# Optimization experiments

Measured on AMD Instinct MI355X. Metric: run time of the kernel, lower is better.

## Reference

```python
import jax, jax.numpy as jnp
import numpy as np

NUM_GROUPS = 8
EPS = 1e-6

def group_norm(x, gamma, beta):
    # x: [B, C, L]
    B, C, L = x.shape
    g = x.reshape(B, NUM_GROUPS, (C // NUM_GROUPS) * L)
    mean = g.mean(axis=-1, keepdims=True)
    var = g.var(axis=-1, keepdims=True)
    g = (g - mean) * jax.lax.rsqrt(var + EPS)
    g = g.reshape(B, C, L)
    return g * gamma[None, :, None] + beta[None, :, None]

def conv1x1(h, w, b):
    # w: [O, C], b: [O]; h: [B, C, L]
    return jnp.einsum('oc,bcl->bol', w, h) + b[None, :, None]

def setup_inputs() -> dict:
    key = jax.random.key(0)
    ks = jax.random.split(key, 12)
    B, C, L = 8, 512, 2048
    s = 1.0 / np.sqrt(C)
    inp = {
        'x': jax.random.normal(ks[0], (B, C, L), dtype=jnp.float32),
        'gamma': jnp.ones((C,), jnp.float32),
        'beta': jnp.zeros((C,), jnp.float32),
        'wq': jax.random.uniform(ks[1], (C, C), jnp.float32, -s, s),
        'bq': jax.random.uniform(ks[2], (C,), jnp.float32, -s, s),
        'wk': jax.random.uniform(ks[3], (C, C), jnp.float32, -s, s),
        'bk': jax.random.uniform(ks[4], (C,), jnp.float32, -s, s),
        'wv': jax.random.uniform(ks[5], (C, C), jnp.float32, -s, s),
        'bv': jax.random.uniform(ks[6], (C,), jnp.float32, -s, s),
        'wo': jax.random.uniform(ks[7], (C, C), jnp.float32, -s, s),
        'bo': jax.random.uniform(ks[8], (C,), jnp.float32, -s, s),
    }
    return inp

def reference(x, gamma, beta, wq, bq, wk, bk, wv, bv, wo, bo):
    C = x.shape[1]
    h = group_norm(x, gamma, beta)
    q = conv1x1(h, wq, bq)  # [B, C, L]
    k = conv1x1(h, wk, bk)
    v = conv1x1(h, wv, bv)
    # scores: [B, Lq, Lk] = q^T k, scaled by C^-0.5
    w = jnp.einsum('bci,bcj->bij', q, k) * (C ** -0.5)
    w = jax.nn.softmax(w, axis=2)
    # h[b,c,i] = sum_j v[b,c,j] * w[b,i,j]
    h = jnp.einsum('bcj,bij->bci', v, w)
    h = conv1x1(h, wo, bo)
    return x + h
```

## Files before the change

kernel.cpp:

```cpp
#include <hip/hip_runtime.h>
#include <hip/hip_bf16.h>
#include <cstdio>

typedef __attribute__((ext_vector_type(8))) short short8;
typedef __attribute__((ext_vector_type(8))) unsigned short ushort8;
typedef __attribute__((ext_vector_type(4))) float f32x4;
typedef __attribute__((ext_vector_type(4))) unsigned short ushort4v;

__device__ inline unsigned short f2bf(float f){
    unsigned int u = __float_as_uint(f);
    unsigned int r = (u + 0x7fffu + ((u >> 16) & 1u)) >> 16;
    return (unsigned short)r;
}
__device__ inline float bf2f(unsigned short b){
    return __uint_as_float((unsigned int)b << 16);
}

__device__ inline void store1(float* p, float v){ *p = v; }
__device__ inline void store1(unsigned short* p, float v){ *p = f2bf(v); }

#define GLDS(gp, lp) __builtin_amdgcn_global_load_lds( \
    (const __attribute__((address_space(1))) void*)(gp), \
    (__attribute__((address_space(3))) void*)(lp), 16, 0, 0)

#define WAITV(N) asm volatile("s_waitcnt vmcnt(" #N ")" ::: "memory")

#define MFMA_Q(ACC, AF, BF) \
    _Pragma("unroll") \
    for (int ks = 0; ks < 2; ks++) \
        _Pragma("unroll") \
        for (int mi = 0; mi < 4; mi++) \
            _Pragma("unroll") \
            for (int ni = 0; ni < 2; ni++) \
                ACC[mi * 2 + ni] = __builtin_amdgcn_mfma_f32_16x16x32_bf16( \
                    AF[ks][mi], BF[ks][ni], ACC[mi * 2 + ni], 0, 0, 0);

template<typename OutT, int EPI>
__global__ __launch_bounds__(512, 2)
void gemm256(const unsigned short* __restrict__ Ag,
             const unsigned short* __restrict__ Bg,
             OutT* __restrict__ Cg,
             int K, int lda, int ldb, int ldc,
             long sA, long sB, long sC,
             const float* __restrict__ bias,
             const float* __restrict__ resid, long sR,
             float scale)
{
    const int gx = gridDim.x, gy = gridDim.y;
    const int nwg  = gx * gy * (int)gridDim.z;
    const int orig = blockIdx.x + gx * (blockIdx.y + gy * blockIdx.z);
    const int cpx  = nwg >> 3;
    const int nid  = (orig & 7) * cpx + (orig >> 3);
    const int bx   = nid % gx;
    const int tmp  = nid / gx;
    const int by   = tmp % gy;
    const int bz   = tmp / gy;

    Ag += (long)bz * sA;
    Bg += (long)bz * sB;
    Cg += (long)bz * sC;
    const int m0 = by * 256;
    const int n0 = bx * 256;

    __shared__ unsigned short As[2][16384];
    __shared__ unsigned short Bs[2][16384];

    const int t    = threadIdx.x;
    const int wave = t >> 6;
    const int lane = t & 63;
    const int rg   = wave >> 2;
    const int cg   = wave & 3;
    const int wm   = rg * 128;
    const int wn   = cg * 64;
    const int lhi  = lane >> 4;
    const int llo  = lane & 15;

    f32x4 acc0[8], acc1[8], acc2[8], acc3[8];
#pragma unroll
    for (int f = 0; f < 8; f++){
        acc0[f] = (f32x4)(0.0f); acc1[f] = (f32x4)(0.0f);
        acc2[f] = (f32x4)(0.0f); acc3[f] = (f32x4)(0.0f);
    }

    const int s_rr = t >> 3, s_cb = t & 7;
    const int s_cs = s_cb ^ (s_rr & 7);
    auto stageA = [&](int bi, int k0, int j){
        GLDS(Ag + (long)(m0 + j * 64 + s_rr) * lda + k0 + s_cs * 8,
             &As[bi][j * 4096 + wave * 512]);
    };
    auto stageB = [&](int bi, int k0, int j){
        GLDS(Bg + (long)(n0 + j * 64 + s_rr) * ldb + k0 + s_cs * 8,
             &Bs[bi][j * 4096 + wave * 512]);
    };

    const int nt = K >> 6;
    stageB(0, 0, 0); stageB(0, 0, 1); stageB(0, 0, 2); stageB(0, 0, 3);
    stageA(0, 0, 0); stageA(0, 0, 2); stageA(0, 0, 1); stageA(0, 0, 3);
    WAITV(2);
    __builtin_amdgcn_s_barrier();
    __builtin_amdgcn_sched_barrier(0);

    int cur = 0;
    for (int kt = 0; kt < nt; kt++){
        const bool more = (kt + 1 < nt);
        const int nk0 = (kt + 1) << 6;
        short8 af[2][4], bf0[2][2], bf1[2][2];

#pragma unroll
        for (int ks = 0; ks < 2; ks++){
#pragma unroll
            for (int mi = 0; mi < 4; mi++){
                const int r  = wm + mi * 16 + llo;
                const int pc = (ks * 4 + lhi) ^ (r & 7);
                af[ks][mi] = *(const short8*)(&As[cur][r * 64 + pc * 8]);
            }
#pragma unroll
            for (int ni = 0; ni < 2; ni++){
                const int r  = wn + ni * 16 + llo;
                const int pc = (ks * 4 + lhi) ^ (r & 7);
                bf0[ks][ni] = *(const short8*)(&Bs[cur][r * 64 + pc * 8]);
            }
        }
        __builtin_amdgcn_sched_barrier(0);
        if (more){ stageB(cur ^ 1, nk0, 0); stageB(cur ^ 1, nk0, 1); }
        __builtin_amdgcn_s_barrier();
        __builtin_amdgcn_sched_barrier(0);
        __builtin_amdgcn_s_setprio(1);
        MFMA_Q(acc0, af, bf0);
        __builtin_amdgcn_s_setprio(0);
        __builtin_amdgcn_s_barrier();
        __builtin_amdgcn_sched_barrier(0);

#pragma unroll
        for (int ks = 0; ks < 2; ks++)
#pragma unroll
            for (int ni = 0; ni < 2; ni++){
                const int r  = wn + 32 + ni * 16 + llo;
                const int pc = (ks * 4 + lhi) ^ (r & 7);
                bf1[ks][ni] = *(const short8*)(&Bs[cur][r * 64 + pc * 8]);
            }
        __builtin_amdgcn_sched_barrier(0);
        if (more){ stageB(cur ^ 1, nk0, 2); stageB(cur ^ 1, nk0, 3); WAITV(4); }
        else     { WAITV(0); }
        __builtin_amdgcn_s_barrier();
        __builtin_amdgcn_sched_barrier(0);
        __builtin_amdgcn_s_setprio(1);
        MFMA_Q(acc1, af, bf1);
        __builtin_amdgcn_s_setprio(0);
        __builtin_amdgcn_s_barrier();
        __builtin_amdgcn_sched_barrier(0);

#pragma unroll
        for (int ks = 0; ks < 2; ks++)
#pragma unroll
            for (int mi = 0; mi < 4; mi++){
                const int r  = wm + 64 + mi * 16 + llo;
                const int pc = (ks * 4 + lhi) ^ (r & 7);
                af[ks][mi] = *(const short8*)(&As[cur][r * 64 + pc * 8]);
            }
        __builtin_amdgcn_sched_barrier(0);
        if (more){ stageA(cur ^ 1, nk0, 0); stageA(cur ^ 1, nk0, 2); }
        __builtin_amdgcn_s_barrier();
        __builtin_amdgcn_sched_barrier(0);
        __builtin_amdgcn_s_setprio(1);
        MFMA_Q(acc2, af, bf1);
        __builtin_amdgcn_s_setprio(0);
        __builtin_amdgcn_s_barrier();
        __builtin_amdgcn_sched_barrier(0);

        if (more){ stageA(cur ^ 1, nk0, 1); stageA(cur ^ 1, nk0, 3); WAITV(2); }
        __builtin_amdgcn_s_barrier();
        __builtin_amdgcn_sched_barrier(0);
        __builtin_amdgcn_s_setprio(1);
        MFMA_Q(acc3, af, bf0);
        __builtin_amdgcn_s_setprio(0);
        __builtin_amdgcn_s_barrier();
        __builtin_amdgcn_sched_barrier(0);

        cur ^= 1;
    }

    auto epi = [&](f32x4 (&A)[8], int h, int cl){
#pragma unroll
        for (int mi = 0; mi < 4; mi++){
#pragma unroll
            for (int ni = 0; ni < 2; ni++){
                const int n  = n0 + wn + cl * 32 + ni * 16 + llo;
                const int mb = m0 + wm + h * 64 + mi * 16 + lhi * 4;
                f32x4 v = A[mi * 2 + ni];
#pragma unroll
                for (int j = 0; j < 4; j++){
                    const int m = mb + j;
                    float val = v[j] * scale;
                    if (EPI == 1) val += bias[n];
                    if (EPI == 2) val += bias[m];
                    if (EPI == 3) val += bias[m] + resid[(long)bz * sR + (long)m * ldc + n];
                    store1(&Cg[(long)m * ldc + n], val);
                }
            }
        }
    };
    epi(acc0, 0, 0); epi(acc1, 0, 1); epi(acc2, 1, 1); epi(acc3, 1, 0);
}

template<typename OutT, int EPI>
__global__ __launch_bounds__(256)
void gemm_nt(const unsigned short* __restrict__ Ag,
             const unsigned short* __restrict__ Bg,
             OutT* __restrict__ Cg,
             int K, int lda, int ldb, int ldc,
             long sA, long sB, long sC,
             const float* __restrict__ bias,
             const float* __restrict__ resid, long sR,
             float scale)
{
    const int gx = gridDim.x, gy = gridDim.y;
    const int nwg  = gx * gy * (int)gridDim.z;
    const int orig = blockIdx.x + gx * (blockIdx.y + gy * blockIdx.z);
    const int cpx  = nwg >> 3;
    const int nid  = (orig & 7) * cpx + (orig >> 3);
    const int bx   = nid % gx;
    const int tmp  = nid / gx;
    const int by   = tmp % gy;
    const int bz   = tmp / gy;

    Ag += (long)bz * sA;
    Bg += (long)bz * sB;
    Cg += (long)bz * sC;
    const int m0 = by * 128;
    const int n0 = bx * 128;

    __shared__ unsigned short As[2][128 * 64];
    __shared__ unsigned short Bs[2][128 * 64];

    const int t    = threadIdx.x;
    const int wave = t >> 6;
    const int lane = t & 63;
    const int wm   = (wave >> 1) << 6;
    const int wn   = (wave & 1) << 6;
    const int lhi  = lane >> 4;
    const int llo  = lane & 15;

    f32x4 acc[4][4];
#pragma unroll
    for (int i = 0; i < 4; i++)
#pragma unroll
        for (int j = 0; j < 4; j++) acc[i][j] = (f32x4)(0.0f);

    auto stage = [&](int bi, int k0){
#pragma unroll
        for (int i = 0; i < 4; i++){
            const int tt = i * 256 + t;
            const int r  = tt >> 3;
            const int cb = tt & 7;
            const int cs = cb ^ (r & 7);
            GLDS(Ag + (long)(m0 + r) * lda + k0 + cs * 8, &As[bi][i * 2048 + wave * 512]);
            GLDS(Bg + (long)(n0 + r) * ldb + k0 + cs * 8, &Bs[bi][i * 2048 + wave * 512]);
        }
    };

    const int nt = K >> 6;
    stage(0, 0);
    __syncthreads();

    int cur = 0;
    for (int kt = 0; kt < nt; kt++){
        if (kt + 1 < nt) stage(cur ^ 1, (kt + 1) << 6);
#pragma unroll
        for (int ksub = 0; ksub < 2; ksub++){
            short8 af[4], bf[4];
#pragma unroll
            for (int mi = 0; mi < 4; mi++){
                const int r  = wm + mi * 16 + llo;
                const int cs = (ksub * 4 + lhi) ^ (r & 7);
                af[mi] = *(const short8*)(&As[cur][r * 64 + cs * 8]);
            }
#pragma unroll
            for (int ni = 0; ni < 4; ni++){
                const int r  = wn + ni * 16 + llo;
                const int cs = (ksub * 4 + lhi) ^ (r & 7);
                bf[ni] = *(const short8*)(&Bs[cur][r * 64 + cs * 8]);
            }
#pragma unroll
            for (int mi = 0; mi < 4; mi++)
#pragma unroll
                for (int ni = 0; ni < 4; ni++)
                    acc[mi][ni] = __builtin_amdgcn_mfma_f32_16x16x32_bf16(
                        af[mi], bf[ni], acc[mi][ni], 0, 0, 0);
        }
        __syncthreads();
        cur ^= 1;
    }

#pragma unroll
    for (int mi = 0; mi < 4; mi++){
#pragma unroll
        for (int ni = 0; ni < 4; ni++){
            const int n  = n0 + wn + ni * 16 + llo;
            const int mb = m0 + wm + mi * 16 + lhi * 4;
            f32x4 v = acc[mi][ni];
#pragma unroll
            for (int j = 0; j < 4; j++){
                const int m = mb + j;
                float val = v[j] * scale;
                if (EPI == 1) val += bias[n];
                if (EPI == 2) val += bias[m];
                if (EPI == 3) val += bias[m] + resid[(long)bz * sR + (long)m * ldc + n];
                store1(&Cg[(long)m * ldc + n], val);
            }
        }
    }
}


__global__ void gn_partial(const float* __restrict__ x, float* __restrict__ part){
    const long base = (long)blockIdx.x * 8192;
    const float4* xp = (const float4*)(x + base);
    float s = 0.f, ss = 0.f;
    for (int i = threadIdx.x; i < 2048; i += 256){
        float4 v = xp[i];
        s  += (v.x + v.y) + (v.z + v.w);
        ss += (v.x * v.x + v.y * v.y) + (v.z * v.z + v.w * v.w);
    }
    for (int o = 32; o; o >>= 1){ s += __shfl_down(s, o); ss += __shfl_down(ss, o); }
    __shared__ float rs[4], rss[4];
    const int wave = threadIdx.x >> 6, lane = threadIdx.x & 63;
    if (lane == 0){ rs[wave] = s; rss[wave] = ss; }
    __syncthreads();
    if (threadIdx.x == 0){
        part[blockIdx.x * 2]     = (rs[0] + rs[1]) + (rs[2] + rs[3]);
        part[blockIdx.x * 2 + 1] = (rss[0] + rss[1]) + (rss[2] + rss[3]);
    }
}

__global__ void gn_final(const float* __restrict__ part, float* __restrict__ stats){
    const int bg = threadIdx.x;
    if (bg >= 64) return;
    float s = 0.f, ss = 0.f;
    for (int c = 0; c < 16; c++){
        s  += part[(bg * 16 + c) * 2];
        ss += part[(bg * 16 + c) * 2 + 1];
    }
    const float inv_n = 1.0f / 131072.0f;
    const float mean = s * inv_n;
    const float var  = ss * inv_n - mean * mean;
    stats[bg * 2]     = mean;
    stats[bg * 2 + 1] = rsqrtf(var + 1e-6f);
}

__global__ void norm_transpose(const float* __restrict__ x, const float* __restrict__ stats,
                               const float* __restrict__ gamma, const float* __restrict__ beta,
                               unsigned short* __restrict__ ht){
    const int b = blockIdx.z, c0 = blockIdx.y * 64, l0 = blockIdx.x * 64;
    const int bg = b * 8 + (c0 >> 6);
    const float mean = stats[bg * 2], rstd = stats[bg * 2 + 1];
    __shared__ unsigned short tile[64][66];
    const float* xb = x + (long)b * 1048576;
    const int t = threadIdx.x;
#pragma unroll
    for (int i = 0; i < 16; i++){
        const int idx = i * 256 + t;
        const int c = idx >> 6, l = idx & 63;
        float v = xb[(long)(c0 + c) * 2048 + l0 + l];
        v = (v - mean) * rstd * gamma[c0 + c] + beta[c0 + c];
        tile[l][c] = f2bf(v);
    }
    __syncthreads();
    unsigned short* htb = ht + (long)b * 1048576;
#pragma unroll
    for (int i = 0; i < 16; i++){
        const int idx = i * 256 + t;
        const int l = idx >> 6, c = idx & 63;
        htb[(long)(l0 + l) * 512 + c0 + c] = tile[l][c];
    }
}

__global__ void weights_to_bf16(const float4* __restrict__ wq, const float4* __restrict__ wk,
                                const float4* __restrict__ wv, const float4* __restrict__ wo,
                                ushort4v* __restrict__ out){
    const int i = blockIdx.x * 256 + threadIdx.x;
    const int w = i >> 16, off = i & 65535;
    const float4* src = (w == 0) ? wq : (w == 1) ? wk : (w == 2) ? wv : wo;
    float4 v = src[off];
    ushort4v o;
    o.x = f2bf(v.x); o.y = f2bf(v.y); o.z = f2bf(v.z); o.w = f2bf(v.w);
    out[i] = o;
}

__global__ void softmax_inplace(unsigned short* __restrict__ p){
    const long base = (long)blockIdx.x * 2048;
    ushort8* pp = (ushort8*)(p + base);
    const int t = threadIdx.x;
    ushort8 v = pp[t];
    float f[8];
#pragma unroll
    for (int j = 0; j < 8; j++) f[j] = bf2f(v[j]);
    float mx = f[0];
#pragma unroll
    for (int j = 1; j < 8; j++) mx = fmaxf(mx, f[j]);
    for (int o = 32; o; o >>= 1) mx = fmaxf(mx, __shfl_xor(mx, o));
    __shared__ float rmax[4], rsum[4];
    const int wave = t >> 6, lane = t & 63;
    if (lane == 0) rmax[wave] = mx;
    __syncthreads();
    mx = fmaxf(fmaxf(rmax[0], rmax[1]), fmaxf(rmax[2], rmax[3]));
    float sum = 0.f;
#pragma unroll
    for (int j = 0; j < 8; j++){ f[j] = __expf(f[j] - mx); sum += f[j]; }
    for (int o = 32; o; o >>= 1) sum += __shfl_xor(sum, o);
    if (lane == 0) rsum[wave] = sum;
    __syncthreads();
    sum = (rsum[0] + rsum[1]) + (rsum[2] + rsum[3]);
    const float inv = 1.0f / sum;
    ushort8 o8;
#pragma unroll
    for (int j = 0; j < 8; j++) o8[j] = f2bf(f[j] * inv);
    pp[t] = o8;
}

enum : long {
    OFF_WQ  = 0,
    OFF_WK  = 524288,
    OFF_WV  = 1048576,
    OFF_WO  = 1572864,
    OFF_HT  = 2097152,
    OFF_QT  = OFF_HT  + 16777216,
    OFF_KT  = OFF_QT  + 16777216,
    OFF_V   = OFF_KT  + 16777216,
    OFF_H2  = OFF_V   + 16777216,
    OFF_P   = OFF_H2  + 16777216,
    OFF_GNP = OFF_P   + 67108864,
    OFF_GNS = OFF_GNP + 8192,
    OFF_END = OFF_GNS + 512
};

extern "C" void kernel_launch(void* const* d_in, const int* in_sizes, int n_in,
                              void* d_out, int out_size, void* d_ws, size_t ws_size,
                              hipStream_t stream)
{
    const float* x     = (const float*)d_in[0];
    const float* gamma = (const float*)d_in[1];
    const float* beta  = (const float*)d_in[2];
    const float* wq    = (const float*)d_in[3];
    const float* bq    = (const float*)d_in[4];
    const float* wk    = (const float*)d_in[5];
    const float* bk    = (const float*)d_in[6];
    const float* wv    = (const float*)d_in[7];
    const float* bv    = (const float*)d_in[8];
    const float* wo    = (const float*)d_in[9];
    const float* bo    = (const float*)d_in[10];
    float* out = (float*)d_out;
    char* ws = (char*)d_ws;

    if (ws_size < (size_t)OFF_END){
        fprintf(stderr, "kernel_launch: ws too small (%zu < %ld)\n", ws_size, (long)OFF_END);
        return;
    }

    unsigned short* HT  = (unsigned short*)(ws + OFF_HT);
    unsigned short* QT  = (unsigned short*)(ws + OFF_QT);
    unsigned short* KT  = (unsigned short*)(ws + OFF_KT);
    unsigned short* V   = (unsigned short*)(ws + OFF_V);
    unsigned short* H2  = (unsigned short*)(ws + OFF_H2);
    unsigned short* P   = (unsigned short*)(ws + OFF_P);
    float*          GNP = (float*)(ws + OFF_GNP);
    float*          GNS = (float*)(ws + OFF_GNS);
    unsigned short* WQb = (unsigned short*)(ws + OFF_WQ);
    unsigned short* WKb = (unsigned short*)(ws + OFF_WK);
    unsigned short* WVb = (unsigned short*)(ws + OFF_WV);
    unsigned short* WOb = (unsigned short*)(ws + OFF_WO);

    const long LC = 1048576;
    const long LL = 4194304;

    weights_to_bf16<<<1024, 256, 0, stream>>>(
        (const float4*)wq, (const float4*)wk, (const float4*)wv, (const float4*)wo,
        (ushort4v*)(ws + OFF_WQ));

    gn_partial<<<1024, 256, 0, stream>>>(x, GNP);
    gn_final<<<1, 64, 0, stream>>>(GNP, GNS);
    norm_transpose<<<dim3(32, 8, 8), 256, 0, stream>>>(x, GNS, gamma, beta, HT);

    gemm_nt<unsigned short, 1><<<dim3(4, 16, 8), 256, 0, stream>>>(
        HT, WQb, QT, 512, 512, 512, 512, LC, 0, LC, bq, nullptr, 0, 1.0f);
    gemm_nt<unsigned short, 1><<<dim3(4, 16, 8), 256, 0, stream>>>(
        HT, WKb, KT, 512, 512, 512, 512, LC, 0, LC, bk, nullptr, 0, 1.0f);
    gemm_nt<unsigned short, 2><<<dim3(16, 4, 8), 256, 0, stream>>>(
        WVb, HT, V, 512, 512, 512, 2048, 0, LC, LC, bv, nullptr, 0, 1.0f);

    gemm256<unsigned short, 0><<<dim3(8, 8, 8), 512, 0, stream>>>(
        QT, KT, P, 512, 512, 512, 2048, LC, LC, LL, nullptr, nullptr, 0, 0.04419417382f);

    softmax_inplace<<<16384, 256, 0, stream>>>(P);

    gemm_nt<unsigned short, 0><<<dim3(4, 16, 8), 256, 0, stream>>>(
        P, V, H2, 2048, 2048, 2048, 512, LL, LC, LC, nullptr, nullptr, 0, 1.0f);

    gemm_nt<float, 3><<<dim3(16, 4, 8), 256, 0, stream>>>(
        WOb, H2, out, 512, 512, 512, 2048, 0, LC, LC, bo, x, LC, 1.0f);
}
```

Baseline: 276.9 us.

## Fuse softmax exp into QK GEMM epilogue and defer normalization to PV GEMM

The QK^T GEMM epilogue now writes exp(score*scale) as bf16 directly. It accumulates per-row sums through lane shuffles, LDS, and global atomics into a zeroed row-sum buffer. The PV GEMM divides its output by that row sum, which removes the separate softmax pass that read and wrote the large score matrix. The Q and K projections are also merged into one GEMM with a concatenated weight and bias, producing an interleaved QK buffer. Dropping max subtraction risks exp overflow for large scores, and the atomics and extra memset add some overhead.

```diff
diff --git a/kernel.cpp b/kernel.cpp
--- a/kernel.cpp
+++ b/kernel.cpp
@@ -43,7 +43,7 @@
              int K, int lda, int ldb, int ldc,
              long sA, long sB, long sC,
              const float* __restrict__ bias,
-             const float* __restrict__ resid, long sR,
+             float* __restrict__ rs, long sRS,
              float scale)
 {
     const int gx = gridDim.x, gy = gridDim.y;
@@ -180,27 +180,84 @@
         cur ^= 1;
     }
 
-    auto epi = [&](f32x4 (&A)[8], int h, int cl){
-#pragma unroll
-        for (int mi = 0; mi < 4; mi++){
-#pragma unroll
-            for (int ni = 0; ni < 2; ni++){
-                const int n  = n0 + wn + cl * 32 + ni * 16 + llo;
-                const int mb = m0 + wm + h * 64 + mi * 16 + lhi * 4;
-                f32x4 v = A[mi * 2 + ni];
+    if constexpr (EPI == 4){
+        float rp[2][4][4];
+#pragma unroll
+        for (int h = 0; h < 2; h++)
+#pragma unroll
+            for (int mi = 0; mi < 4; mi++)
+#pragma unroll
+                for (int j = 0; j < 4; j++) rp[h][mi][j] = 0.0f;
+
+        auto epi4 = [&](f32x4 (&A)[8], int h, int cl){
+#pragma unroll
+            for (int mi = 0; mi < 4; mi++)
+#pragma unroll
+                for (int ni = 0; ni < 2; ni++){
+                    const int n  = n0 + wn + cl * 32 + ni * 16 + llo;
+                    const int mb = m0 + wm + h * 64 + mi * 16 + lhi * 4;
+                    f32x4 v = A[mi * 2 + ni];
+#pragma unroll
+                    for (int j = 0; j < 4; j++){
+                        float e = __expf(v[j] * scale);
+                        unsigned short b = f2bf(e);
+                        Cg[(long)(mb + j) * ldc + n] = b;
+                        rp[h][mi][j] += bf2f(b);
+                    }
+                }
+        };
+        epi4(acc0, 0, 0); epi4(acc1, 0, 1); epi4(acc2, 1, 1); epi4(acc3, 1, 0);
+
+#pragma unroll
+        for (int h = 0; h < 2; h++)
+#pragma unroll
+            for (int mi = 0; mi < 4; mi++)
 #pragma unroll
                 for (int j = 0; j < 4; j++){
-                    const int m = mb + j;
-                    float val = v[j] * scale;
-                    if (EPI == 1) val += bias[n];
-                    if (EPI == 2) val += bias[m];
-                    if (EPI == 3) val += bias[m] + resid[(long)bz * sR + (long)m * ldc + n];
-                    store1(&Cg[(long)m * ldc + n], val);
+                    float v = rp[h][mi][j];
+                    v += __shfl_xor(v, 1);
+                    v += __shfl_xor(v, 2);
+                    v += __shfl_xor(v, 4);
+                    v += __shfl_xor(v, 8);
+                    rp[h][mi][j] = v;
                 }
-            }
+        __syncthreads();
+        float* LDSr = (float*)&As[0][0];
+        if (llo == 0){
+#pragma unroll
+            for (int h = 0; h < 2; h++)
+#pragma unroll
+                for (int mi = 0; mi < 4; mi++)
+#pragma unroll
+                    for (int j = 0; j < 4; j++)
+                        LDSr[(rg * 128 + h * 64 + mi * 16 + lhi * 4 + j) * 4 + cg]
+                            = rp[h][mi][j];
         }
-    };
-    epi(acc0, 0, 0); epi(acc1, 0, 1); epi(acc2, 1, 1); epi(acc3, 1, 0);
+        __syncthreads();
+        if (t < 256){
+            float s = (LDSr[t * 4 + 0] + LDSr[t * 4 + 1])
+                    + (LDSr[t * 4 + 2] + LDSr[t * 4 + 3]);
+            atomicAdd(&rs[(long)bz * sRS + m0 + t], s);
+        }
+    } else {
+        auto epi = [&](f32x4 (&A)[8], int h, int cl){
+#pragma unroll
+            for (int mi = 0; mi < 4; mi++)
+#pragma unroll
+                for (int ni = 0; ni < 2; ni++){
+                    const int n  = n0 + wn + cl * 32 + ni * 16 + llo;
+                    const int mb = m0 + wm + h * 64 + mi * 16 + lhi * 4;
+                    f32x4 v = A[mi * 2 + ni];
+#pragma unroll
+                    for (int j = 0; j < 4; j++){
+                        float val = v[j] * scale;
+                        if (EPI == 1) val += bias[n];
+                        store1(&Cg[(long)(mb + j) * ldc + n], val);
+                    }
+                }
+        };
+        epi(acc0, 0, 0); epi(acc1, 0, 1); epi(acc2, 1, 1); epi(acc3, 1, 0);
+    }
 }
 
 template<typename OutT, int EPI>
@@ -212,6 +269,7 @@
              long sA, long sB, long sC,
              const float* __restrict__ bias,
              const float* __restrict__ resid, long sR,
+             const float* __restrict__ rs, long sRS,
              float scale)
 {
     const int gx = gridDim.x, gy = gridDim.y;
@@ -306,6 +364,7 @@
                 if (EPI == 1) val += bias[n];
                 if (EPI == 2) val += bias[m];
                 if (EPI == 3) val += bias[m] + resid[(long)bz * sR + (long)m * ldc + n];
+                if (EPI == 5) val /= rs[(long)bz * sRS + m];
                 store1(&Cg[(long)m * ldc + n], val);
             }
         }
@@ -323,12 +382,12 @@
         ss += (v.x * v.x + v.y * v.y) + (v.z * v.z + v.w * v.w);
     }
     for (int o = 32; o; o >>= 1){ s += __shfl_down(s, o); ss += __shfl_down(ss, o); }
-    __shared__ float rs[4], rss[4];
+    __shared__ float rsd[4], rss[4];
     const int wave = threadIdx.x >> 6, lane = threadIdx.x & 63;
-    if (lane == 0){ rs[wave] = s; rss[wave] = ss; }
+    if (lane == 0){ rsd[wave] = s; rss[wave] = ss; }
     __syncthreads();
     if (threadIdx.x == 0){
-        part[blockIdx.x * 2]     = (rs[0] + rs[1]) + (rs[2] + rs[3]);
+        part[blockIdx.x * 2]     = (rsd[0] + rsd[1]) + (rsd[2] + rsd[3]);
         part[blockIdx.x * 2 + 1] = (rss[0] + rss[1]) + (rss[2] + rss[3]);
     }
 }
@@ -377,56 +436,29 @@
 
 __global__ void weights_to_bf16(const float4* __restrict__ wq, const float4* __restrict__ wk,
                                 const float4* __restrict__ wv, const float4* __restrict__ wo,
-                                ushort4v* __restrict__ out){
+                                const float* __restrict__ bq, const float* __restrict__ bk,
+                                ushort4v* __restrict__ out, float* __restrict__ bqk){
     const int i = blockIdx.x * 256 + threadIdx.x;
-    const int w = i >> 16, off = i & 65535;
-    const float4* src = (w == 0) ? wq : (w == 1) ? wk : (w == 2) ? wv : wo;
-    float4 v = src[off];
-    ushort4v o;
-    o.x = f2bf(v.x); o.y = f2bf(v.y); o.z = f2bf(v.z); o.w = f2bf(v.w);
-    out[i] = o;
-}
-
-__global__ void softmax_inplace(unsigned short* __restrict__ p){
-    const long base = (long)blockIdx.x * 2048;
-    ushort8* pp = (ushort8*)(p + base);
-    const int t = threadIdx.x;
-    ushort8 v = pp[t];
-    float f[8];
-#pragma unroll
-    for (int j = 0; j < 8; j++) f[j] = bf2f(v[j]);
-    float mx = f[0];
-#pragma unroll
-    for (int j = 1; j < 8; j++) mx = fmaxf(mx, f[j]);
-    for (int o = 32; o; o >>= 1) mx = fmaxf(mx, __shfl_xor(mx, o));
-    __shared__ float rmax[4], rsum[4];
-    const int wave = t >> 6, lane = t & 63;
-    if (lane == 0) rmax[wave] = mx;
-    __syncthreads();
-    mx = fmaxf(fmaxf(rmax[0], rmax[1]), fmaxf(rmax[2], rmax[3]));
-    float sum = 0.f;
-#pragma unroll
-    for (int j = 0; j < 8; j++){ f[j] = __expf(f[j] - mx); sum += f[j]; }
-    for (int o = 32; o; o >>= 1) sum += __shfl_xor(sum, o);
-    if (lane == 0) rsum[wave] = sum;
-    __syncthreads();
-    sum = (rsum[0] + rsum[1]) + (rsum[2] + rsum[3]);
-    const float inv = 1.0f / sum;
-    ushort8 o8;
-#pragma unroll
-    for (int j = 0; j < 8; j++) o8[j] = f2bf(f[j] * inv);
-    pp[t] = o8;
+    if (i < 262144){
+        const int w = i >> 16, off = i & 65535;
+        const float4* src = (w == 0) ? wq : (w == 1) ? wk : (w == 2) ? wv : wo;
+        float4 v = src[off];
+        ushort4v o;
+        o.x = f2bf(v.x); o.y = f2bf(v.y); o.z = f2bf(v.z); o.w = f2bf(v.w);
+        out[i] = o;
+    } else {
+        const int j = i - 262144;
+        if (j < 1024) bqk[j] = (j < 512) ? bq[j] : bk[j - 512];
+    }
 }
 
 enum : long {
     OFF_WQ  = 0,
-    OFF_WK  = 524288,
-    OFF_WV  = 1048576,
-    OFF_WO  = 1572864,
-    OFF_HT  = 2097152,
-    OFF_QT  = OFF_HT  + 16777216,
-    OFF_KT  = OFF_QT  + 16777216,
-    OFF_V   = OFF_KT  + 16777216,
+    OFF_BQK = 2097152,
+    OFF_RS  = OFF_BQK + 4096,
+    OFF_HT  = OFF_RS  + 65536,
+    OFF_QK  = OFF_HT  + 16777216,
+    OFF_V   = OFF_QK  + 33554432,
     OFF_H2  = OFF_V   + 16777216,
     OFF_P   = OFF_H2  + 16777216,
     OFF_GNP = OFF_P   + 67108864,
@@ -457,45 +489,45 @@
         return;
     }
 
+    unsigned short* WQb = (unsigned short*)(ws + OFF_WQ);
+    unsigned short* WVb = WQb + 2 * 262144;
+    unsigned short* WOb = WQb + 3 * 262144;
+    float*          BQK = (float*)(ws + OFF_BQK);
+    float*          RS  = (float*)(ws + OFF_RS);
     unsigned short* HT  = (unsigned short*)(ws + OFF_HT);
-    unsigned short* QT  = (unsigned short*)(ws + OFF_QT);
-    unsigned short* KT  = (unsigned short*)(ws + OFF_KT);
+    unsigned short* QK  = (unsigned short*)(ws + OFF_QK);
     unsigned short* V   = (unsigned short*)(ws + OFF_V);
     unsigned short* H2  = (unsigned short*)(ws + OFF_H2);
     unsigned short* P   = (unsigned short*)(ws + OFF_P);
     float*          GNP = (float*)(ws + OFF_GNP);
     float*          GNS = (float*)(ws + OFF_GNS);
-    unsigned short* WQb = (unsigned short*)(ws + OFF_WQ);
-    unsigned short* WKb = (unsigned short*)(ws + OFF_WK);
-    unsigned short* WVb = (unsigned short*)(ws + OFF_WV);
-    unsigned short* WOb = (unsigned short*)(ws + OFF_WO);
-
-    const long LC = 1048576;
-    const long LL = 4194304;
-
-    weights_to_bf16<<<1024, 256, 0, stream>>>(
+
+    const long LC  = 1048576;
+    const long LQK = 2097152;
+    const long LL  = 4194304;
+
+    hipMemsetAsync(RS, 0, 65536, stream);
+
+    weights_to_bf16<<<1028, 256, 0, stream>>>(
         (const float4*)wq, (const float4*)wk, (const float4*)wv, (const float4*)wo,
-        (ushort4v*)(ws + OFF_WQ));
+        bq, bk, (ushort4v*)WQb, BQK);
 
     gn_partial<<<1024, 256, 0, stream>>>(x, GNP);
     gn_final<<<1, 64, 0, stream>>>(GNP, GNS);
     norm_transpose<<<dim3(32, 8, 8), 256, 0, stream>>>(x, GNS, gamma, beta, HT);
 
-    gemm_nt<unsigned short, 1><<<dim3(4, 16, 8), 256, 0, stream>>>(
-        HT, WQb, QT, 512, 512, 512, 512, LC, 0, LC, bq, nullptr, 0, 1.0f);
-    gemm_nt<unsigned short, 1><<<dim3(4, 16, 8), 256, 0, stream>>>(
-        HT, WKb, KT, 512, 512, 512, 512, LC, 0, LC, bk, nullptr, 0, 1.0f);
+    gemm_nt<unsigned short, 1><<<dim3(8, 16, 8), 256, 0, stream>>>(
+        HT, WQb, QK, 512, 512, 512, 1024, LC, 0, LQK, BQK, nullptr, 0, nullptr, 0, 1.0f);
     gemm_nt<unsigned short, 2><<<dim3(16, 4, 8), 256, 0, stream>>>(
-        WVb, HT, V, 512, 512, 512, 2048, 0, LC, LC, bv, nullptr, 0, 1.0f);
-
-    gemm256<unsigned short, 0><<<dim3(8, 8, 8), 512, 0, stream>>>(
-        QT, KT, P, 512, 512, 512, 2048, LC, LC, LL, nullptr, nullptr, 0, 0.04419417382f);
-
-    softmax_inplace<<<16384, 256, 0, stream>>>(P);
-
-    gemm_nt<unsigned short, 0><<<dim3(4, 16, 8), 256, 0, stream>>>(
-        P, V, H2, 2048, 2048, 2048, 512, LL, LC, LC, nullptr, nullptr, 0, 1.0f);
+        WVb, HT, V, 512, 512, 512, 2048, 0, LC, LC, bv, nullptr, 0, nullptr, 0, 1.0f);
+
+    gemm256<unsigned short, 4><<<dim3(8, 8, 8), 512, 0, stream>>>(
+        QK, QK + 512, P, 512, 1024, 1024, 2048, LQK, LQK, LL,
+        nullptr, RS, 2048, 0.04419417382f);
+
+    gemm_nt<unsigned short, 5><<<dim3(4, 16, 8), 256, 0, stream>>>(
+        P, V, H2, 2048, 2048, 2048, 512, LL, LC, LC, nullptr, nullptr, 0, RS, 2048, 1.0f);
 
     gemm_nt<float, 3><<<dim3(16, 4, 8), 256, 0, stream>>>(
-        WOb, H2, out, 512, 512, 512, 2048, 0, LC, LC, bo, x, LC, 1.0f);
-}
+        WOb, H2, out, 512, 512, 512, 2048, 0, LC, LC, bo, x, LC, nullptr, 0, 1.0f);
+}
```

Result: faster. 270.0 us (-2.5%).
